# Performance work log

Measured on AMD Instinct MI355X. Metric: run time of the kernel, lower is better.

Reference implementation:

```python
import jax, jax.numpy as jnp
import numpy as np


def _slim_scale(out_c, wvec, dtype):
    # SlimConv2d splits output channels at 0.6/0.7/0.8/0.9 and scales splits 1..4
    # by weights[1..4] (split 0 is unscaled). Equivalent to one conv + channel scale.
    c0, c1, c2, c3 = int(0.6 * out_c), int(0.7 * out_c), int(0.8 * out_c), int(0.9 * out_c)
    return jnp.concatenate([
        jnp.ones((c0,), dtype),
        wvec[1] * jnp.ones((c1 - c0,), dtype),
        wvec[2] * jnp.ones((c2 - c1,), dtype),
        wvec[3] * jnp.ones((c3 - c2,), dtype),
        wvec[4] * jnp.ones((out_c - c3,), dtype),
    ])


def _slim_conv(x, W, b, pad_t, wvec):
    # x: (N,C,T,V), W: (O,I,kT,kV)
    y = jax.lax.conv_general_dilated(
        x, W, window_strides=(1, 1), padding=((pad_t, pad_t), (0, 0)),
        dimension_numbers=('NCHW', 'OIHW', 'NCHW'))
    y = y + b[None, :, None, None]
    scale = _slim_scale(W.shape[0], wvec, x.dtype)
    return y * scale[None, :, None, None]


def setup_inputs() -> dict:
    key = jax.random.key(0)
    ks = jax.random.split(key, 8)
    N, C, T, V = 64, 64, 300, 25
    S, IC = 3, 16  # num_subset, inter_channels = 64 // 4
    x = jax.random.normal(ks[0], (N, C, T, V), jnp.float32)
    weights = jax.random.uniform(ks[1], (5,), jnp.float32)
    A = jax.random.uniform(ks[2], (S, V, V), jnp.float32) * 0.1
    PA = jnp.full((S, V, V), 1e-6, jnp.float32)
    Wd = jax.random.normal(ks[3], (S, C, C, 1, 1), jnp.float32) * (2.0 / (C * 3)) ** 0.5
    bd = jnp.zeros((S, C), jnp.float32)
    WT1 = jax.random.normal(ks[4], (S, IC, C, 9, 1), jnp.float32) * 0.05
    bT1 = jnp.zeros((S, IC), jnp.float32)
    WT2 = jax.random.normal(ks[5], (S, IC, C, 9, 1), jnp.float32) * 0.05
    bT2 = jnp.zeros((S, IC), jnp.float32)
    bn_gamma = jnp.ones((C,), jnp.float32)
    bn_beta = jnp.zeros((C,), jnp.float32)
    bn_mean = jnp.zeros((C,), jnp.float32)
    bn_var = jnp.ones((C,), jnp.float32)
    return dict(x=x, weights=weights, A=A, PA=PA, Wd=Wd, bd=bd, WT1=WT1, bT1=bT1,
                WT2=WT2, bT2=bT2, bn_gamma=bn_gamma, bn_beta=bn_beta,
                bn_mean=bn_mean, bn_var=bn_var)


def reference(x, weights, A, PA, Wd, bd, WT1, bT1, WT2, bT2,
              bn_gamma, bn_beta, bn_mean, bn_var):
    N, C, T, V = x.shape
    inter_c = WT1.shape[1]
    num_subset = A.shape[0]
    # Chebyshev-like adjacency term: 8A^4 - 4A^2 - 4A + I (elementwise powers)
    A_ch = 8 * A ** 4 - 4 * A ** 2 - 4 * A + jnp.eye(V, dtype=A.dtype)
    A_full = A + PA + A_ch  # (S, V, V)
    y = None
    for i in range(num_subset):
        t1 = _slim_conv(x, WT1[i], bT1[i], 4, weights)  # (N, inter_c, T, V)
        t2 = _slim_conv(x, WT2[i], bT2[i], 4, weights)  # (N, inter_c, T, V)
        q = t1.transpose(0, 3, 1, 2).reshape(N, V, inter_c * T)  # (N, V, IC*T)
        k = t2.reshape(N, inter_c * T, V)                          # (N, IC*T, V)
        att = jax.nn.softmax(jnp.matmul(q, k) / (inter_c * T), axis=-2)  # (N, V, V)
        A1 = A_full[i] + att
        agg = jnp.matmul(x.reshape(N, C * T, V), A1).reshape(N, C, T, V)
        z = _slim_conv(agg, Wd[i], bd[i], 0, weights)
        y = z if y is None else y + z
    # BatchNorm2d in eval mode
    inv = jax.lax.rsqrt(bn_var + 1e-5)
    y = (y - bn_mean[None, :, None, None]) * (bn_gamma * inv)[None, :, None, None] \
        + bn_beta[None, :, None, None]
    y = y + x  # down is identity since in_channels == out_channels
    return jax.nn.relu(y)
```

## Files before the change

### kernel.cpp

```cpp
#include <hip/hip_runtime.h>

constexpr int N_ = 64, C_ = 64, T_ = 300, V_ = 25, IC_ = 16, S_ = 3, KT_ = 9;

constexpr int TP_   = T_ + 12;

constexpr int TTM   = 16;
constexpr int SROWS = TTM + 8;
constexpr int MROWS = SROWS * V_;
constexpr int CSTR  = 32;
constexpr int NTB   = (T_ + TTM - 1) / TTM;
constexpr int KS_   = 266;

constexpr int TTZ   = 16;
constexpr int NTBZ  = (T_ + TTZ - 1) / TTZ;
constexpr int ASTR  = 36;

typedef __bf16 bf16x8 __attribute__((ext_vector_type(8)));
typedef __bf16 bf16x4 __attribute__((ext_vector_type(4)));
typedef float  f32x4  __attribute__((ext_vector_type(4)));

constexpr int OFF_AFULL = 0;
constexpr int SZ_AFULL  = S_ * V_ * V_;
constexpr int OFF_WTB   = OFF_AFULL + SZ_AFULL;
constexpr int SZ_WTB_F  = (S_ * KT_ * 32 * C_) / 2;
constexpr int OFF_BTC   = OFF_WTB + SZ_WTB_F;
constexpr int OFF_WDB   = OFF_BTC + S_ * 32;
constexpr int SZ_WDB_F  = (S_ * C_ * C_) / 2;
constexpr int OFF_BDT   = OFF_WDB + SZ_WDB_F;
constexpr int OFF_BNA   = OFF_BDT + C_;
constexpr int OFF_BNB   = OFF_BNA + C_;
constexpr int OFF_A1    = OFF_BNB + C_;
constexpr int SZ_A1     = S_ * N_ * V_ * V_;
constexpr int OFF_SACC  = OFF_A1 + SZ_A1;
constexpr int SZ_SACC   = S_ * N_ * V_ * V_;

__device__ __forceinline__ float slim16(const float* w, int o) {
    if (o < 9)  return 1.0f;
    if (o < 11) return w[1];
    if (o < 12) return w[2];
    if (o < 14) return w[3];
    return w[4];
}
__device__ __forceinline__ float slim64(const float* w, int o) {
    if (o < 38) return 1.0f;
    if (o < 44) return w[1];
    if (o < 51) return w[2];
    if (o < 57) return w[3];
    return w[4];
}

__global__ void prep_kernel(const float* __restrict__ x,   __bf16* __restrict__ xt,
                            const float* __restrict__ wv,  const float* __restrict__ A,
                            const float* __restrict__ PA,  const float* __restrict__ Wd,
                            const float* __restrict__ bd,  const float* __restrict__ WT1,
                            const float* __restrict__ bT1, const float* __restrict__ WT2,
                            const float* __restrict__ bT2, const float* __restrict__ gam,
                            const float* __restrict__ bet, const float* __restrict__ mu,
                            const float* __restrict__ var, float* __restrict__ ws)
{
    const int gid = blockIdx.x * blockDim.x + threadIdx.x;
    const int stride = gridDim.x * blockDim.x;
    for (int idx = gid; idx < N_ * TP_ * V_ * 8; idx += stride) {
        const int cg = idx & 7;
        const int v  = (idx >> 3) % V_;
        const int tt = (idx / (V_ * 8)) % TP_;
        const int n  = idx / (V_ * 8 * TP_);
        const int t  = tt - 4;
        bf16x8 pk;
        if (t >= 0 && t < T_) {
            const float* gp = x + ((size_t)(n * C_ + cg * 8) * T_ + t) * V_ + v;
#pragma unroll
            for (int jj = 0; jj < 8; ++jj) pk[jj] = (__bf16)gp[(size_t)jj * T_ * V_];
        } else {
#pragma unroll
            for (int jj = 0; jj < 8; ++jj) pk[jj] = (__bf16)0.f;
        }
        *(bf16x8*)&xt[((size_t)(n * TP_ + tt) * V_ + v) * C_ + cg * 8] = pk;
    }
    for (int idx = gid; idx < SZ_SACC; idx += stride)
        ws[OFF_SACC + idx] = 0.f;
    for (int idx = gid; idx < S_ * V_ * V_; idx += stride) {
        int uv = idx % (V_ * V_);
        int u = uv / V_, v = uv % V_;
        float a  = A[idx];
        float a2 = a * a;
        ws[OFF_AFULL + idx] = a + PA[idx] + 8.f * a2 * a2 - 4.f * a2 - 4.f * a
                              + (u == v ? 1.f : 0.f);
    }
    {
        __bf16* wtb = (__bf16*)(ws + OFF_WTB);
        for (int idx = gid; idx < S_ * KT_ * 32 * C_; idx += stride) {
            int c  = idx % C_;
            int r  = idx / C_;
            int o  = r % 32;  r /= 32;
            int kt = r % KT_;
            int i  = r / KT_;
            float val;
            if (o < IC_)
                val = slim16(wv, o) * WT1[((i * IC_ + o) * C_ + c) * KT_ + kt];
            else
                val = slim16(wv, o - IC_) * WT2[((i * IC_ + (o - IC_)) * C_ + c) * KT_ + kt];
            wtb[idx] = (__bf16)val;
        }
    }
    for (int idx = gid; idx < S_ * 32; idx += stride) {
        int i = idx / 32, o = idx % 32;
        float val = (o < IC_) ? slim16(wv, o) * bT1[i * IC_ + o]
                              : slim16(wv, o - IC_) * bT2[i * IC_ + (o - IC_)];
        ws[OFF_BTC + idx] = val;
    }
    {
        __bf16* wdb = (__bf16*)(ws + OFF_WDB);
        for (int idx = gid; idx < S_ * C_ * C_; idx += stride) {
            int c = idx % C_;
            int o = (idx / C_) % C_;
            int i = idx / (C_ * C_);
            wdb[idx] = (__bf16)(slim64(wv, o) * Wd[(i * C_ + o) * C_ + c]);
        }
    }
    for (int idx = gid; idx < C_; idx += stride) {
        float bt = 0.f;
        for (int i = 0; i < S_; ++i) bt += slim64(wv, idx) * bd[i * C_ + idx];
        ws[OFF_BDT + idx] = bt;
        float ba = gam[idx] * rsqrtf(var[idx] + 1e-5f);
        ws[OFF_BNA + idx] = ba;
        ws[OFF_BNB + idx] = bet[idx] - mu[idx] * ba;
    }
}

__global__ __launch_bounds__(320) void tconv_att_kernel(
    const __bf16* __restrict__ xt, const __bf16* __restrict__ wt,
    const float* __restrict__ btc, float* __restrict__ sacc)
{
    __shared__ __align__(16) char lds_raw[MROWS * CSTR * 2];
    __bf16* xs  = (__bf16*)lds_raw;
    __bf16* t1L = (__bf16*)lds_raw;
    __bf16* t2L = t1L + 32 * KS_;
    const int tid  = threadIdx.x;
    const int n    = blockIdx.y;
    const int t0   = blockIdx.x * TTM;
    const int wv   = tid >> 6;
    const int lane = tid & 63;
    const int l15  = lane & 15;
    const int quad = lane >> 4;

    f32x4 acc[5][6];
#pragma unroll
    for (int j = 0; j < 5; ++j)
#pragma unroll
        for (int p = 0; p < 6; ++p) acc[j][p] = (f32x4){0.f, 0.f, 0.f, 0.f};

    for (int ch = 0; ch < 2; ++ch) {
        const int c0 = ch * 32;
        __syncthreads();
        {
            const __bf16* xtb = xt + (size_t)(n * TP_ + t0) * (V_ * C_) + c0;
            for (int idx = tid; idx < MROWS * 4; idx += 320) {
                const int lr = idx >> 2, cg = idx & 3;
                const bf16x8 pk = *(const bf16x8*)&xtb[lr * C_ + cg * 8];
                *(bf16x8*)&xs[idx * 8] = pk;
            }
        }
        __syncthreads();

        for (int kt = 0; kt < KT_; ++kt) {
            bf16x8 a[6];
#pragma unroll
            for (int p = 0; p < 6; ++p) {
                const int i = p >> 1, h = p & 1;
                a[p] = *(const bf16x8*)&wt[((size_t)((i * KT_ + kt) * 32 + h * 16 + l15)) * C_ + c0 + quad * 8];
            }
#pragma unroll
            for (int j = 0; j < 5; ++j) {
                const int r = (wv * 5 + j) * 16 + l15 + V_ * kt;
                const bf16x8 b = *(const bf16x8*)&xs[r * CSTR + quad * 8];
#pragma unroll
                for (int p = 0; p < 6; ++p)
                    acc[j][p] = __builtin_amdgcn_mfma_f32_16x16x32_bf16(a[p], b, acc[j][p], 0, 0, 0);
            }
        }
    }

    for (int i = 0; i < S_; ++i) {
        __syncthreads();
#pragma unroll
        for (int j = 0; j < 5; ++j) {
            const int m  = (wv * 5 + j) * 16 + l15;
            const int tl = m / V_;
            const int u  = m % V_;
            const bool valid = (t0 + tl) < T_;
#pragma unroll
            for (int h = 0; h < 2; ++h) {
                bf16x4 pk;
#pragma unroll
                for (int r = 0; r < 4; ++r) {
                    const float val = valid
                        ? (acc[j][i * 2 + h][r] + btc[i * 32 + h * 16 + quad * 4 + r])
                        : 0.f;
                    pk[r] = (__bf16)val;
                }
                *(bf16x4*)((h ? t2L : t1L) + u * KS_ + tl * 16 + quad * 4) = pk;
            }
        }
        __syncthreads();
        if (wv < 4) {
            const int ut = wv >> 1, vt = wv & 1;
            f32x4 sa = (f32x4){0.f, 0.f, 0.f, 0.f};
#pragma unroll
            for (int ks = 0; ks < 8; ++ks) {
                const bf16x8 A = *(const bf16x8*)&t1L[(ut * 16 + l15) * KS_ + ks * 32 + quad * 8];
                const bf16x8 B = *(const bf16x8*)&t2L[(vt * 16 + l15) * KS_ + ks * 32 + quad * 8];
                sa = __builtin_amdgcn_mfma_f32_16x16x32_bf16(A, B, sa, 0, 0, 0);
            }
            float* sp = sacc + ((size_t)i * N_ + n) * (V_ * V_);
#pragma unroll
            for (int r = 0; r < 4; ++r) {
                const int u = ut * 16 + quad * 4 + r;
                const int v = vt * 16 + l15;
                if (u < V_ && v < V_) atomicAdd(&sp[u * V_ + v], sa[r]);
            }
        }
    }
}

__global__ __launch_bounds__(256) void att_softmax_kernel(
    const float* __restrict__ sacc, const float* __restrict__ afull,
    float* __restrict__ a1o)
{
    __shared__ float Ss[V_ * V_];
    const int n = blockIdx.x;
    const int i = blockIdx.y;
    const int tid = threadIdx.x;
    for (int p = tid; p < V_ * V_; p += 256)
        Ss[p] = sacc[((size_t)i * N_ + n) * (V_ * V_) + p] * (1.0f / (IC_ * T_));
    __syncthreads();
    if (tid < V_) {
        const int v = tid;
        float m = -1e30f;
#pragma unroll
        for (int u = 0; u < V_; ++u) m = fmaxf(m, Ss[u * V_ + v]);
        float e[V_]; float es = 0.f;
#pragma unroll
        for (int u = 0; u < V_; ++u) { e[u] = expf(Ss[u * V_ + v] - m); es += e[u]; }
        const float inv = 1.0f / es;
#pragma unroll
        for (int u = 0; u < V_; ++u)
            a1o[((size_t)i * N_ + n) * (V_ * V_) + u * V_ + v]
                = afull[i * (V_ * V_) + u * V_ + v] + e[u] * inv;
    }
}

__global__ __launch_bounds__(320) void agg_out_mfma_kernel(
    const float* __restrict__ x,   const float* __restrict__ a1,
    const __bf16* __restrict__ wdb, const float* __restrict__ bdt,
    const float* __restrict__ bna, const float* __restrict__ bnb,
    float* __restrict__ out)
{
    __shared__ __align__(16) __bf16 ags[400 * ASTR];
    __shared__ __align__(16) __bf16 a1t3[S_ * 32 * 32];
    const int tid  = threadIdx.x;
    const int n    = blockIdx.y;
    const int t0   = blockIdx.x * TTZ;
    const int wv   = tid >> 6;
    const int lane = tid & 63;
    const int l15  = lane & 15;
    const int quad = lane >> 4;

    for (int idx = tid; idx < S_ * 1024; idx += 320) {
        const int i = idx >> 10;
        const int r = idx & 1023;
        const int v = r >> 5, u = r & 31;
        float val = (v < V_ && u < V_)
                  ? a1[((size_t)(i * N_ + n) * V_ + u) * V_ + v] : 0.f;
        a1t3[idx] = (__bf16)val;
    }

    f32x4 acc[5][4];
#pragma unroll
    for (int j = 0; j < 5; ++j)
#pragma unroll
        for (int ot = 0; ot < 4; ++ot) acc[j][ot] = (f32x4){0.f, 0.f, 0.f, 0.f};

    const int tg = t0 + l15;
    for (int chunk = 0; chunk < 2; ++chunk) {
        const int c0 = chunk * 32;
        bf16x8 afr[7];
#pragma unroll
        for (int k = 0; k < 7; ++k) {
            const int c = wv + 5 * k;
            bf16x8 pk;
#pragma unroll
            for (int jj = 0; jj < 8; ++jj) pk[jj] = (__bf16)0.f;
            if (c < 32 && tg < T_) {
                const float* gp = x + ((size_t)(n * C_ + c0 + c) * T_ + tg) * V_;
#pragma unroll
                for (int jj = 0; jj < 8; ++jj) {
                    const int u = quad * 8 + jj;
                    if (u < V_) pk[jj] = (__bf16)gp[u];
                }
            }
            afr[k] = pk;
        }
        for (int i = 0; i < S_; ++i) {
            __syncthreads();
            const bf16x8 b0 = *(const bf16x8*)&a1t3[i * 1024 + l15 * 32 + quad * 8];
            const bf16x8 b1 = *(const bf16x8*)&a1t3[i * 1024 + (16 + l15) * 32 + quad * 8];
#pragma unroll
            for (int k = 0; k < 7; ++k) {
                const int c = wv + 5 * k;
                if (c < 32) {
                    f32x4 d0 = (f32x4){0.f, 0.f, 0.f, 0.f};
                    f32x4 d1 = (f32x4){0.f, 0.f, 0.f, 0.f};
                    d0 = __builtin_amdgcn_mfma_f32_16x16x32_bf16(afr[k], b0, d0, 0, 0, 0);
                    d1 = __builtin_amdgcn_mfma_f32_16x16x32_bf16(afr[k], b1, d1, 0, 0, 0);
#pragma unroll
                    for (int r = 0; r < 4; ++r) {
                        const int tl = quad * 4 + r;
                        ags[(tl * V_ + l15) * ASTR + c] = (__bf16)d0[r];
                        if (l15 < V_ - 16)
                            ags[(tl * V_ + 16 + l15) * ASTR + c] = (__bf16)d1[r];
                    }
                }
            }
            __syncthreads();
            bf16x8 bw[4];
#pragma unroll
            for (int ot = 0; ot < 4; ++ot)
                bw[ot] = *(const bf16x8*)&wdb[(size_t)(i * C_ + ot * 16 + l15) * C_ + c0 + quad * 8];
#pragma unroll
            for (int j = 0; j < 5; ++j) {
                const int m2 = (wv * 5 + j) * 16 + l15;
                const bf16x4 lo = *(const bf16x4*)&ags[m2 * ASTR + quad * 8];
                const bf16x4 hi = *(const bf16x4*)&ags[m2 * ASTR + quad * 8 + 4];
                const bf16x8 am = __builtin_shufflevector(lo, hi, 0, 1, 2, 3, 4, 5, 6, 7);
#pragma unroll
                for (int ot = 0; ot < 4; ++ot)
                    acc[j][ot] = __builtin_amdgcn_mfma_f32_16x16x32_bf16(am, bw[ot], acc[j][ot], 0, 0, 0);
            }
        }
    }

    const int mrem = (T_ - t0) * V_;
#pragma unroll
    for (int ot = 0; ot < 4; ++ot) {
        const int o  = ot * 16 + l15;
        const float ba = bna[o], bb = bnb[o], bt = bdt[o];
#pragma unroll
        for (int j = 0; j < 5; ++j) {
            const int m2b = (wv * 5 + j) * 16 + quad * 4;
            if (m2b + 3 < mrem) {
                const size_t gi = (size_t)(n * C_ + o) * (T_ * V_) + (size_t)t0 * V_ + m2b;
                const f32x4 xr = *(const f32x4*)&x[gi];
                f32x4 rs;
#pragma unroll
                for (int r = 0; r < 4; ++r)
                    rs[r] = fmaxf(fmaf(acc[j][ot][r] + bt, ba, bb) + xr[r], 0.f);
                *(f32x4*)&out[gi] = rs;
            }
        }
    }
}

extern "C" void kernel_launch(void* const* d_in, const int* in_sizes, int n_in,
                              void* d_out, int out_size, void* d_ws, size_t ws_size,
                              hipStream_t stream)
{
    (void)in_sizes; (void)n_in; (void)out_size; (void)ws_size;
    const float* x    = (const float*)d_in[0];
    const float* wv   = (const float*)d_in[1];
    const float* A    = (const float*)d_in[2];
    const float* PA   = (const float*)d_in[3];
    const float* Wd   = (const float*)d_in[4];
    const float* bd   = (const float*)d_in[5];
    const float* WT1  = (const float*)d_in[6];
    const float* bT1  = (const float*)d_in[7];
    const float* WT2  = (const float*)d_in[8];
    const float* bT2  = (const float*)d_in[9];
    const float* gam  = (const float*)d_in[10];
    const float* bet  = (const float*)d_in[11];
    const float* mu   = (const float*)d_in[12];
    const float* var  = (const float*)d_in[13];
    float* ws  = (float*)d_ws;
    float* out = (float*)d_out;

    __bf16* xt = (__bf16*)d_out;

    prep_kernel<<<dim3(15600), dim3(256), 0, stream>>>(
        x, xt, wv, A, PA, Wd, bd, WT1, bT1, WT2, bT2, gam, bet, mu, var, ws);

    tconv_att_kernel<<<dim3(NTB, N_), dim3(320), 0, stream>>>(
        xt, (const __bf16*)(ws + OFF_WTB), ws + OFF_BTC, ws + OFF_SACC);

    att_softmax_kernel<<<dim3(N_, S_), dim3(256), 0, stream>>>(
        ws + OFF_SACC, ws + OFF_AFULL, ws + OFF_A1);

    agg_out_mfma_kernel<<<dim3(NTBZ, N_), dim3(320), 0, stream>>>(
        x, ws + OFF_A1, (const __bf16*)(ws + OFF_WDB),
        ws + OFF_BDT, ws + OFF_BNA, ws + OFF_BNB, out);
}
```

Before: 568.8 us.

## Tile x transpose through LDS in prep and double-buffer aggregation stage

The prep kernel now converts x to the padded channel-last bf16 layout by staging 10-timestep tiles in shared memory. Reads become contiguous float2 loads instead of loads strided across channels. A small set of extra blocks zero-fills the padding rows and does the weight and adjacency prep. The aggregation kernel double-buffers its shared staging tile so the per-subset projection of step k overlaps the output MFMA of step k-1, halving barriers, and its row stride shrinks from 36 to 34. The odd stride may make the 8-byte LDS vector reads misaligned.

```diff
diff --git a/kernel.cpp b/kernel.cpp
--- a/kernel.cpp
+++ b/kernel.cpp
@@ -3,6 +3,11 @@
 constexpr int N_ = 64, C_ = 64, T_ = 300, V_ = 25, IC_ = 16, S_ = 3, KT_ = 9;
 
 constexpr int TP_   = T_ + 12;
+
+constexpr int TCH   = 10;
+constexpr int NTCH  = T_ / TCH;
+constexpr int NTR   = N_ * NTCH;
+constexpr int LTR   = 251;
 
 constexpr int TTM   = 16;
 constexpr int SROWS = TTM + 8;
@@ -13,7 +18,7 @@
 
 constexpr int TTZ   = 16;
 constexpr int NTBZ  = (T_ + TTZ - 1) / TTZ;
-constexpr int ASTR  = 36;
+constexpr int ASTR  = 34;
 
 typedef __bf16 bf16x8 __attribute__((ext_vector_type(8)));
 typedef __bf16 bf16x4 __attribute__((ext_vector_type(4)));
@@ -49,33 +54,54 @@
     return w[4];
 }
 
-__global__ void prep_kernel(const float* __restrict__ x,   __bf16* __restrict__ xt,
-                            const float* __restrict__ wv,  const float* __restrict__ A,
-                            const float* __restrict__ PA,  const float* __restrict__ Wd,
-                            const float* __restrict__ bd,  const float* __restrict__ WT1,
-                            const float* __restrict__ bT1, const float* __restrict__ WT2,
-                            const float* __restrict__ bT2, const float* __restrict__ gam,
-                            const float* __restrict__ bet, const float* __restrict__ mu,
-                            const float* __restrict__ var, float* __restrict__ ws)
+__global__ __launch_bounds__(256) void prep_kernel(
+    const float* __restrict__ x,   __bf16* __restrict__ xt,
+    const float* __restrict__ wv,  const float* __restrict__ A,
+    const float* __restrict__ PA,  const float* __restrict__ Wd,
+    const float* __restrict__ bd,  const float* __restrict__ WT1,
+    const float* __restrict__ bT1, const float* __restrict__ WT2,
+    const float* __restrict__ bT2, const float* __restrict__ gam,
+    const float* __restrict__ bet, const float* __restrict__ mu,
+    const float* __restrict__ var, float* __restrict__ ws)
 {
-    const int gid = blockIdx.x * blockDim.x + threadIdx.x;
-    const int stride = gridDim.x * blockDim.x;
-    for (int idx = gid; idx < N_ * TP_ * V_ * 8; idx += stride) {
+    __shared__ __bf16 tl_[C_ * LTR];
+    const int tid = threadIdx.x;
+
+    if (blockIdx.x < NTR) {
+        const int n   = blockIdx.x / NTCH;
+        const int t0g = (blockIdx.x % NTCH) * TCH;
+        for (int idx = tid; idx < C_ * 125; idx += 256) {
+            const int c = idx / 125;
+            const int w = idx % 125;
+            const float2 val = *(const float2*)&x[((size_t)(n * C_ + c) * T_ + t0g) * V_ + w * 2];
+            tl_[c * LTR + w * 2]     = (__bf16)val.x;
+            tl_[c * LTR + w * 2 + 1] = (__bf16)val.y;
+        }
+        __syncthreads();
+        for (int idx = tid; idx < 250 * 8; idx += 256) {
+            const int cg = idx & 7;
+            const int tv = idx >> 3;
+            bf16x8 pk;
+#pragma unroll
+            for (int jj = 0; jj < 8; ++jj) pk[jj] = tl_[(cg * 8 + jj) * LTR + tv];
+            const int dt = tv / V_, v = tv % V_;
+            *(bf16x8*)&xt[((size_t)(n * TP_ + t0g + 4 + dt) * V_ + v) * C_ + cg * 8] = pk;
+        }
+        return;
+    }
+
+    const int gid = (blockIdx.x - NTR) * 256 + tid;
+    const int stride = 64 * 256;
+    for (int idx = gid; idx < N_ * 12 * V_ * 8; idx += stride) {
         const int cg = idx & 7;
         const int v  = (idx >> 3) % V_;
-        const int tt = (idx / (V_ * 8)) % TP_;
-        const int n  = idx / (V_ * 8 * TP_);
-        const int t  = tt - 4;
-        bf16x8 pk;
-        if (t >= 0 && t < T_) {
-            const float* gp = x + ((size_t)(n * C_ + cg * 8) * T_ + t) * V_ + v;
-#pragma unroll
-            for (int jj = 0; jj < 8; ++jj) pk[jj] = (__bf16)gp[(size_t)jj * T_ * V_];
-        } else {
-#pragma unroll
-            for (int jj = 0; jj < 8; ++jj) pk[jj] = (__bf16)0.f;
-        }
-        *(bf16x8*)&xt[((size_t)(n * TP_ + tt) * V_ + v) * C_ + cg * 8] = pk;
+        const int hr = (idx / (8 * V_)) % 12;
+        const int n  = idx / (8 * V_ * 12);
+        const int tt = (hr < 4) ? hr : 300 + hr;
+        bf16x8 z;
+#pragma unroll
+        for (int jj = 0; jj < 8; ++jj) z[jj] = (__bf16)0.f;
+        *(bf16x8*)&xt[((size_t)(n * TP_ + tt) * V_ + v) * C_ + cg * 8] = z;
     }
     for (int idx = gid; idx < SZ_SACC; idx += stride)
         ws[OFF_SACC + idx] = 0.f;
@@ -256,7 +282,7 @@
     const float* __restrict__ bna, const float* __restrict__ bnb,
     float* __restrict__ out)
 {
-    __shared__ __align__(16) __bf16 ags[400 * ASTR];
+    __shared__ __align__(16) __bf16 ags[2][400 * ASTR];
     __shared__ __align__(16) __bf16 a1t3[S_ * 32 * 32];
     const int tid  = threadIdx.x;
     const int n    = blockIdx.y;
@@ -282,62 +308,70 @@
         for (int ot = 0; ot < 4; ++ot) acc[j][ot] = (f32x4){0.f, 0.f, 0.f, 0.f};
 
     const int tg = t0 + l15;
-    for (int chunk = 0; chunk < 2; ++chunk) {
-        const int c0 = chunk * 32;
-        bf16x8 afr[7];
-#pragma unroll
-        for (int k = 0; k < 7; ++k) {
-            const int c = wv + 5 * k;
-            bf16x8 pk;
-#pragma unroll
-            for (int jj = 0; jj < 8; ++jj) pk[jj] = (__bf16)0.f;
-            if (c < 32 && tg < T_) {
-                const float* gp = x + ((size_t)(n * C_ + c0 + c) * T_ + tg) * V_;
-#pragma unroll
-                for (int jj = 0; jj < 8; ++jj) {
-                    const int u = quad * 8 + jj;
-                    if (u < V_) pk[jj] = (__bf16)gp[u];
+    bf16x8 afr[7];
+    __syncthreads();
+
+    for (int k = 0; k <= 6; ++k) {
+        if (k < 6) {
+            const int ch = k / 3, i = k - ch * 3, c0 = ch * 32;
+            if (i == 0) {
+#pragma unroll
+                for (int kk = 0; kk < 7; ++kk) {
+                    const int c = wv + 5 * kk;
+                    bf16x8 pk;
+#pragma unroll
+                    for (int jj = 0; jj < 8; ++jj) pk[jj] = (__bf16)0.f;
+                    if (c < 32 && tg < T_) {
+                        const float* gp = x + ((size_t)(n * C_ + c0 + c) * T_ + tg) * V_;
+#pragma unroll
+                        for (int jj = 0; jj < 8; ++jj) {
+                            const int u = quad * 8 + jj;
+                            if (u < V_) pk[jj] = (__bf16)gp[u];
+                        }
+                    }
+                    afr[kk] = pk;
                 }
             }
-            afr[k] = pk;
-        }
-        for (int i = 0; i < S_; ++i) {
-            __syncthreads();
+            __bf16* aw = &ags[k & 1][0];
             const bf16x8 b0 = *(const bf16x8*)&a1t3[i * 1024 + l15 * 32 + quad * 8];
             const bf16x8 b1 = *(const bf16x8*)&a1t3[i * 1024 + (16 + l15) * 32 + quad * 8];
 #pragma unroll
-            for (int k = 0; k < 7; ++k) {
-                const int c = wv + 5 * k;
+            for (int kk = 0; kk < 7; ++kk) {
+                const int c = wv + 5 * kk;
                 if (c < 32) {
                     f32x4 d0 = (f32x4){0.f, 0.f, 0.f, 0.f};
                     f32x4 d1 = (f32x4){0.f, 0.f, 0.f, 0.f};
-                    d0 = __builtin_amdgcn_mfma_f32_16x16x32_bf16(afr[k], b0, d0, 0, 0, 0);
-                    d1 = __builtin_amdgcn_mfma_f32_16x16x32_bf16(afr[k], b1, d1, 0, 0, 0);
+                    d0 = __builtin_amdgcn_mfma_f32_16x16x32_bf16(afr[kk], b0, d0, 0, 0, 0);
+                    d1 = __builtin_amdgcn_mfma_f32_16x16x32_bf16(afr[kk], b1, d1, 0, 0, 0);
 #pragma unroll
                     for (int r = 0; r < 4; ++r) {
                         const int tl = quad * 4 + r;
-                        ags[(tl * V_ + l15) * ASTR + c] = (__bf16)d0[r];
+                        aw[(tl * V_ + l15) * ASTR + c] = (__bf16)d0[r];
                         if (l15 < V_ - 16)
-                            ags[(tl * V_ + 16 + l15) * ASTR + c] = (__bf16)d1[r];
+                            aw[(tl * V_ + 16 + l15) * ASTR + c] = (__bf16)d1[r];
                     }
                 }
             }
-            __syncthreads();
+        }
+        if (k > 0) {
+            const int kp = k - 1, chp = kp / 3, ip = kp - chp * 3, c0p = chp * 32;
+            const __bf16* ar = &ags[kp & 1][0];
             bf16x8 bw[4];
 #pragma unroll
             for (int ot = 0; ot < 4; ++ot)
-                bw[ot] = *(const bf16x8*)&wdb[(size_t)(i * C_ + ot * 16 + l15) * C_ + c0 + quad * 8];
+                bw[ot] = *(const bf16x8*)&wdb[(size_t)(ip * C_ + ot * 16 + l15) * C_ + c0p + quad * 8];
 #pragma unroll
             for (int j = 0; j < 5; ++j) {
                 const int m2 = (wv * 5 + j) * 16 + l15;
-                const bf16x4 lo = *(const bf16x4*)&ags[m2 * ASTR + quad * 8];
-                const bf16x4 hi = *(const bf16x4*)&ags[m2 * ASTR + quad * 8 + 4];
+                const bf16x4 lo = *(const bf16x4*)&ar[m2 * ASTR + quad * 8];
+                const bf16x4 hi = *(const bf16x4*)&ar[m2 * ASTR + quad * 8 + 4];
                 const bf16x8 am = __builtin_shufflevector(lo, hi, 0, 1, 2, 3, 4, 5, 6, 7);
 #pragma unroll
                 for (int ot = 0; ot < 4; ++ot)
                     acc[j][ot] = __builtin_amdgcn_mfma_f32_16x16x32_bf16(am, bw[ot], acc[j][ot], 0, 0, 0);
             }
         }
+        if (k < 6) __syncthreads();
     }
 
     const int mrem = (T_ - t0) * V_;
@@ -385,7 +419,7 @@
 
     __bf16* xt = (__bf16*)d_out;
 
-    prep_kernel<<<dim3(15600), dim3(256), 0, stream>>>(
+    prep_kernel<<<dim3(NTR + 64), dim3(256), 0, stream>>>(
         x, xt, wv, A, PA, Wd, bd, WT1, bT1, WT2, bT2, gam, bet, mu, var, ws);
 
     tconv_att_kernel<<<dim3(NTB, N_), dim3(320), 0, stream>>>(
```

After: 604.1 us. 6.2% more time.
